# Kernel optimization log

Measured on AMD Instinct MI355X. Metric: run time of the kernel, lower is better.

The kernel has to match this reference:

```python
import jax, jax.numpy as jnp
import numpy as np

S, B, E, H = 2048, 2, 1024, 16
D = E // H  # head dim = 64


def setup_inputs() -> dict:
    key = jax.random.key(0)
    k1, k2, k3 = jax.random.split(key, 3)
    x = jax.random.normal(k1, (S, B, E), dtype=jnp.float32)
    Wqkv = jax.random.normal(k2, (3 * E, E), dtype=jnp.float32) * (E ** -0.5)
    bqkv = jax.random.normal(k3, (3 * E,), dtype=jnp.float32) * 0.02
    return {"x": x, "Wqkv": Wqkv, "bqkv": bqkv}


def reference(x, Wqkv, bqkv):
    s, b, e = x.shape
    h, d = H, E // H
    # fused QKV projection: [S,B,E] @ [E,3E] -> [S,B,3E]
    qkv = jnp.einsum('sbe,fe->sbf', x, Wqkv) + bqkv
    q, k, v = jnp.split(qkv, 3, axis=-1)
    q = q.reshape(s, b, h, d)
    k = k.reshape(s, b, h, d)
    v = v.reshape(s, b, h, d)
    scale = 1.0 / jnp.sqrt(jnp.asarray(d, dtype=x.dtype))
    # scores: [B,H,S,S]
    scores = jnp.einsum('sbhd,tbhd->bhst', q, k) * scale
    attn = jax.nn.softmax(scores, axis=-1)
    # context: [S,B,H,D] -> [S,B,E]
    ctx = jnp.einsum('bhst,tbhd->sbhd', attn, v)
    return ctx.reshape(s, b, e)
```

## Files before the change

### kernel.cpp

```cpp
#include <hip/hip_runtime.h>

constexpr int SEQ   = 2048;
constexpr int BATCH = 2;
constexpr int EMB   = 1024;
constexpr int NH    = 16;
constexpr int HDIM  = 64;
constexpr int MROWS = SEQ * BATCH;
constexpr int KDIM  = EMB;
constexpr int NCOLS = 3 * EMB;

typedef __bf16 bf16x8 __attribute__((ext_vector_type(8)));
typedef __bf16 bf16x4 __attribute__((ext_vector_type(4)));
typedef float  f32x4  __attribute__((ext_vector_type(4)));
typedef float  f32x16 __attribute__((ext_vector_type(16)));
typedef unsigned int u32;
typedef unsigned int u32x4 __attribute__((ext_vector_type(4)));

__device__ __forceinline__ u32 cvt_pk_bf16(float lo, float hi) {
  u32 r;
  asm("v_cvt_pk_bf16_f32 %0, %1, %2" : "=v"(r) : "v"(lo), "v"(hi));
  return r;
}
__device__ __forceinline__ void pl32_swap(u32& a, u32& b) {
  asm("v_permlane32_swap_b32 %0, %1" : "+v"(a), "+v"(b));
}
__device__ __forceinline__ void g2l16(const __bf16* g, __bf16* l) {
  __builtin_amdgcn_global_load_lds(
      (const __attribute__((address_space(1))) void*)g,
      (__attribute__((address_space(3))) void*)l, 16, 0, 0);
}

__global__ __launch_bounds__(256) void cvt_f32_bf16(
    const float* __restrict__ src, __bf16* __restrict__ dst, int n4) {
  int stride = gridDim.x * blockDim.x;
  for (int i = blockIdx.x * blockDim.x + threadIdx.x; i < n4; i += stride) {
    float4 v = reinterpret_cast<const float4*>(src)[i];
    bf16x4 o;
    o[0] = (__bf16)v.x; o[1] = (__bf16)v.y; o[2] = (__bf16)v.z; o[3] = (__bf16)v.w;
    reinterpret_cast<bf16x4*>(dst)[i] = o;
  }
}

__global__ __launch_bounds__(256) void qkv_gemm(
    const __bf16* __restrict__ Xb, const __bf16* __restrict__ Wb,
    const float* __restrict__ bqkv,
    __bf16* __restrict__ Qb, __bf16* __restrict__ Kb, __bf16* __restrict__ Vt) {
  __shared__ __attribute__((aligned(16))) __bf16 Al[128 * 64];
  __shared__ __attribute__((aligned(16))) __bf16 Bl[128 * 64];

  const int tid  = threadIdx.x;
  const int lane = tid & 63;
  const int w    = tid >> 6;
  const int wm   = w >> 1, wn = w & 1;
  const int m0   = blockIdx.y * 128;
  const int n0   = blockIdx.x * 128;

  f32x4 acc[4][4] = {};

  for (int kt = 0; kt < KDIM / 64; ++kt) {
    const int k0 = kt * 64;
    __syncthreads();
#pragma unroll
    for (int c = 0; c < 4; ++c) {
      const int u   = (w * 4 + c) * 64 + lane;
      const int row = u >> 3;
      const int sc  = ((u & 7) * 8) ^ ((row & 7) << 3);
      g2l16(&Xb[(size_t)(m0 + row) * KDIM + k0 + sc], Al + (w * 4 + c) * 512);
      g2l16(&Wb[(size_t)(n0 + row) * KDIM + k0 + sc], Bl + (w * 4 + c) * 512);
    }
    __syncthreads();

#pragma unroll
    for (int s = 0; s < 2; ++s) {
      bf16x8 af[4], bfr[4];
#pragma unroll
      for (int i = 0; i < 4; ++i) {
        const int ra = wm * 64 + i * 16 + (lane & 15);
        const int rb = wn * 64 + i * 16 + (lane & 15);
        const int colb = s * 32 + (lane >> 4) * 8;
        af[i]  = *reinterpret_cast<const bf16x8*>(&Al[ra * 64 + (colb ^ ((ra & 7) << 3))]);
        bfr[i] = *reinterpret_cast<const bf16x8*>(&Bl[rb * 64 + (colb ^ ((rb & 7) << 3))]);
      }
#pragma unroll
      for (int i = 0; i < 4; ++i)
#pragma unroll
        for (int j = 0; j < 4; ++j)
          acc[i][j] = __builtin_amdgcn_mfma_f32_16x16x32_bf16(af[i], bfr[j], acc[i][j], 0, 0, 0);
    }
  }

  const float QSCALE = 0.18033688011112042f;
#pragma unroll
  for (int j = 0; j < 4; ++j) {
    const int f    = n0 + wn * 64 + j * 16 + (lane & 15);
    const float bias = bqkv[f];
    const int sec  = f >> 10;
    const int hd   = f & 1023;
    const int h    = hd >> 6, d = hd & 63;
#pragma unroll
    for (int i = 0; i < 4; ++i) {
#pragma unroll
      for (int r = 0; r < 4; ++r) {
        const int mm = m0 + wm * 64 + i * 16 + (lane >> 4) * 4 + r;
        const int s_ = mm >> 1, b_ = mm & 1;
        const int bh = b_ * NH + h;
        const float val = acc[i][j][r] + bias;
        if (sec == 0) {
          Qb[((size_t)bh * SEQ + s_) * HDIM + d] = (__bf16)(val * QSCALE);
        } else if (sec == 1) {
          Kb[((size_t)bh * SEQ + s_) * HDIM + d] = (__bf16)val;
        } else {
          Vt[((size_t)bh * HDIM + d) * SEQ + s_] = (__bf16)val;
        }
      }
    }
  }
}

__global__ __launch_bounds__(256) void attn_fwd(
    const __bf16* __restrict__ Qb, const __bf16* __restrict__ Kb,
    const __bf16* __restrict__ Vt, float* __restrict__ out) {
  __shared__ __attribute__((aligned(16))) __bf16 lds[16384];

  const int tid  = threadIdx.x;
  const int lane = tid & 63;
  const int w    = tid >> 6;
  const int lq   = lane & 31;
  const int hi   = lane >> 5;

  const int bid  = blockIdx.x;
  const int wgid = (bid & 7) * 64 + (bid >> 3);
  const int qi   = wgid & 15;
  const int bh   = wgid >> 4;
  const int b_   = bh >> 4, h = bh & 15;
  const int q0   = qi * 128 + w * 32;

  const __bf16* Qp = Qb + (size_t)bh * SEQ * HDIM;
  const __bf16* Kp = Kb + (size_t)bh * SEQ * HDIM;
  const __bf16* Vp = Vt + (size_t)bh * HDIM * SEQ;

  bf16x8 qf[4];
#pragma unroll
  for (int ks = 0; ks < 4; ++ks)
    qf[ks] = *reinterpret_cast<const bf16x8*>(&Qp[(size_t)(q0 + lq) * HDIM + ks * 16 + hi * 8]);

  f32x16 acc0 = {}, acc1 = {};
  float m = -1e30f, l = 0.f;

  auto stage = [&](int b, int t0) {
#pragma unroll
    for (int c = 0; c < 2; ++c) {
      const int u   = (w * 2 + c) * 64 + lane;
      const int row = u >> 3;
      const int sc  = ((u & 7) * 8) ^ ((row & 7) << 3);
      g2l16(Kp + (size_t)(t0 + row) * HDIM + sc, lds + b * 8192 + (w * 2 + c) * 512);
      g2l16(Vp + (size_t)row * SEQ + t0 + sc,    lds + b * 8192 + 4096 + (w * 2 + c) * 512);
    }
  };

  stage(0, 0);
  __syncthreads();
  int cur = 0;

  for (int t0 = 0; t0 < SEQ; t0 += 64) {
    if (t0 + 64 < SEQ) stage(cur ^ 1, t0 + 64);
    const __bf16* kb = lds + cur * 8192;
    const __bf16* vb = kb + 4096;

    f32x16 S0 = {}, S1 = {};
#pragma unroll
    for (int ks = 0; ks < 4; ++ks) {
      const int colb = ks * 16 + hi * 8;
      bf16x8 k0 = *reinterpret_cast<const bf16x8*>(&kb[lq * 64        + (colb ^ ((lq & 7) << 3))]);
      bf16x8 k1 = *reinterpret_cast<const bf16x8*>(&kb[(32 + lq) * 64 + (colb ^ ((lq & 7) << 3))]);
      S0 = __builtin_amdgcn_mfma_f32_32x32x16_bf16(k0, qf[ks], S0, 0, 0, 0);
      S1 = __builtin_amdgcn_mfma_f32_32x32x16_bf16(k1, qf[ks], S1, 0, 0, 0);
    }

    float pmax = S0[0];
#pragma unroll
    for (int i = 1; i < 16; ++i) pmax = fmaxf(pmax, S0[i]);
#pragma unroll
    for (int i = 0; i < 16; ++i) pmax = fmaxf(pmax, S1[i]);
    pmax = fmaxf(pmax, __shfl_xor(pmax, 32));
    const float mnew  = fmaxf(m, pmax);
    const float alpha = __builtin_amdgcn_exp2f(m - mnew);
    m = mnew;
    float rs = 0.f;
#pragma unroll
    for (int i = 0; i < 16; ++i) { S0[i] = __builtin_amdgcn_exp2f(S0[i] - mnew); rs += S0[i]; }
#pragma unroll
    for (int i = 0; i < 16; ++i) { S1[i] = __builtin_amdgcn_exp2f(S1[i] - mnew); rs += S1[i]; }
    l = l * alpha + rs;
#pragma unroll
    for (int i = 0; i < 16; ++i) { acc0[i] *= alpha; acc1[i] *= alpha; }

    bf16x8 pw[4];
    {
      auto mk = [&](const f32x16& P, bf16x8* dst) {
#pragma unroll
        for (int kk = 0; kk < 2; ++kk) {
          u32 a0 = cvt_pk_bf16(P[kk * 8 + 0], P[kk * 8 + 1]);
          u32 b0 = cvt_pk_bf16(P[kk * 8 + 4], P[kk * 8 + 5]);
          u32 a1 = cvt_pk_bf16(P[kk * 8 + 2], P[kk * 8 + 3]);
          u32 b1 = cvt_pk_bf16(P[kk * 8 + 6], P[kk * 8 + 7]);
          pl32_swap(a0, b0);
          pl32_swap(a1, b1);
          u32x4 wv; wv[0] = a0; wv[1] = a1; wv[2] = b0; wv[3] = b1;
          dst[kk] = __builtin_bit_cast(bf16x8, wv);
        }
      };
      mk(S0, &pw[0]);
      mk(S1, &pw[2]);
    }

#pragma unroll
    for (int ks = 0; ks < 4; ++ks) {
      const int colb = ks * 16 + hi * 8;
      bf16x8 v0 = *reinterpret_cast<const bf16x8*>(&vb[lq * 64        + (colb ^ ((lq & 7) << 3))]);
      bf16x8 v1 = *reinterpret_cast<const bf16x8*>(&vb[(32 + lq) * 64 + (colb ^ ((lq & 7) << 3))]);
      acc0 = __builtin_amdgcn_mfma_f32_32x32x16_bf16(v0, pw[ks], acc0, 0, 0, 0);
      acc1 = __builtin_amdgcn_mfma_f32_32x32x16_bf16(v1, pw[ks], acc1, 0, 0, 0);
    }

    __syncthreads();
    cur ^= 1;
  }

  l += __shfl_xor(l, 32);
  const float inv = 1.0f / l;
  const int s_ = q0 + lq;
  float* op = out + ((size_t)s_ * BATCH + b_) * EMB + h * HDIM;
#pragma unroll
  for (int rr = 0; rr < 4; ++rr) {
    float4 o0 = {acc0[4 * rr] * inv, acc0[4 * rr + 1] * inv,
                 acc0[4 * rr + 2] * inv, acc0[4 * rr + 3] * inv};
    *reinterpret_cast<float4*>(&op[8 * rr + 4 * hi]) = o0;
    float4 o1 = {acc1[4 * rr] * inv, acc1[4 * rr + 1] * inv,
                 acc1[4 * rr + 2] * inv, acc1[4 * rr + 3] * inv};
    *reinterpret_cast<float4*>(&op[8 * rr + 4 * hi + 32]) = o1;
  }
}

extern "C" void kernel_launch(void* const* d_in, const int* in_sizes, int n_in,
                              void* d_out, int out_size, void* d_ws, size_t ws_size,
                              hipStream_t stream) {
  (void)in_sizes; (void)n_in; (void)out_size; (void)ws_size;
  const float* x    = (const float*)d_in[0];
  const float* Wqkv = (const float*)d_in[1];
  const float* bias = (const float*)d_in[2];
  float* out = (float*)d_out;

  char* ws = (char*)d_ws;
  __bf16* Xb = (__bf16*)(ws);
  __bf16* Wb = (__bf16*)(ws + 8388608);
  __bf16* Qb = (__bf16*)(ws + 14680064);
  __bf16* Kb = (__bf16*)(ws + 23068672);
  __bf16* Vt = (__bf16*)(ws + 31457280);

  cvt_f32_bf16<<<dim3(1024), dim3(256), 0, stream>>>(x, Xb, (MROWS * KDIM) / 4);
  cvt_f32_bf16<<<dim3(768), dim3(256), 0, stream>>>(Wqkv, Wb, (NCOLS * KDIM) / 4);
  qkv_gemm<<<dim3(NCOLS / 128, MROWS / 128), dim3(256), 0, stream>>>(Xb, Wb, bias, Qb, Kb, Vt);
  attn_fwd<<<dim3(512), dim3(256), 0, stream>>>(Qb, Kb, Vt, out);
}
```

Before: 126.1 us.

## Double-buffer QKV GEMM, shrink attention blocks, add lazy rescale and priorities

The QKV GEMM now uses a double-buffered 32-wide K loop with a new LDS swizzle, XCD-aware block remapping, setprio around MFMAs, and a single barrier per iteration. Attention moves to 128-thread blocks covering 64 queries, giving 1024 blocks with each wave staging more of K/V. It also adds setprio around the MFMA phases, tree max/sum reductions, and a lazy max rescale that skips the alpha update unless the max grows by more than 8 (log2 units). The goal is better load/compute overlap and more occupancy. Smaller attention blocks double K/V LDS traffic per query, and the lazy rescale lets exponents reach up to 2^8 before the correction is applied.

```diff
diff --git a/kernel.cpp b/kernel.cpp
--- a/kernel.cpp
+++ b/kernel.cpp
@@ -41,58 +41,68 @@
   }
 }
 
-__global__ __launch_bounds__(256) void qkv_gemm(
+__global__ __launch_bounds__(256, 4) void qkv_gemm(
     const __bf16* __restrict__ Xb, const __bf16* __restrict__ Wb,
     const float* __restrict__ bqkv,
     __bf16* __restrict__ Qb, __bf16* __restrict__ Kb, __bf16* __restrict__ Vt) {
-  __shared__ __attribute__((aligned(16))) __bf16 Al[128 * 64];
-  __shared__ __attribute__((aligned(16))) __bf16 Bl[128 * 64];
+  __shared__ __attribute__((aligned(16))) __bf16 Al[2][128 * 32];
+  __shared__ __attribute__((aligned(16))) __bf16 Bl[2][128 * 32];
 
   const int tid  = threadIdx.x;
   const int lane = tid & 63;
   const int w    = tid >> 6;
   const int wm   = w >> 1, wn = w & 1;
-  const int m0   = blockIdx.y * 128;
-  const int n0   = blockIdx.x * 128;
+
+  const int bid  = blockIdx.x;
+  const int wgid = (bid & 7) * 96 + (bid >> 3);
+  const int nx   = wgid % 24;
+  const int nyy  = wgid / 24;
+  const int m0   = nyy * 128;
+  const int n0   = nx * 128;
 
   f32x4 acc[4][4] = {};
 
-  for (int kt = 0; kt < KDIM / 64; ++kt) {
-    const int k0 = kt * 64;
+  auto stage = [&](int buf, int kt) {
+#pragma unroll
+    for (int c = 0; c < 2; ++c) {
+      const int u   = (w * 2 + c) * 64 + lane;
+      const int row = u >> 2;
+      const int sc  = ((u & 3) ^ ((row >> 1) & 3)) * 8;
+      g2l16(&Xb[(size_t)(m0 + row) * KDIM + kt * 32 + sc], &Al[buf][(w * 2 + c) * 512]);
+      g2l16(&Wb[(size_t)(n0 + row) * KDIM + kt * 32 + sc], &Bl[buf][(w * 2 + c) * 512]);
+    }
+  };
+
+  stage(0, 0);
+  __syncthreads();
+
+  const int l15 = lane & 15, hi4 = lane >> 4;
+  const int cswz = (hi4 ^ ((l15 >> 1) & 3)) * 8;
+
+  for (int kt = 0; kt < KDIM / 32; ++kt) {
+    const int buf = kt & 1;
+    if (kt + 1 < KDIM / 32) stage(buf ^ 1, kt + 1);
+
+    bf16x8 af[4], bfr[4];
+#pragma unroll
+    for (int i = 0; i < 4; ++i) {
+      af[i]  = *reinterpret_cast<const bf16x8*>(&Al[buf][(wm * 64 + i * 16 + l15) * 32 + cswz]);
+      bfr[i] = *reinterpret_cast<const bf16x8*>(&Bl[buf][(wn * 64 + i * 16 + l15) * 32 + cswz]);
+    }
+    __builtin_amdgcn_s_setprio(1);
+#pragma unroll
+    for (int i = 0; i < 4; ++i)
+#pragma unroll
+      for (int j = 0; j < 4; ++j)
+        acc[i][j] = __builtin_amdgcn_mfma_f32_16x16x32_bf16(af[i], bfr[j], acc[i][j], 0, 0, 0);
+    __builtin_amdgcn_s_setprio(0);
     __syncthreads();
-#pragma unroll
-    for (int c = 0; c < 4; ++c) {
-      const int u   = (w * 4 + c) * 64 + lane;
-      const int row = u >> 3;
-      const int sc  = ((u & 7) * 8) ^ ((row & 7) << 3);
-      g2l16(&Xb[(size_t)(m0 + row) * KDIM + k0 + sc], Al + (w * 4 + c) * 512);
-      g2l16(&Wb[(size_t)(n0 + row) * KDIM + k0 + sc], Bl + (w * 4 + c) * 512);
-    }
-    __syncthreads();
-
-#pragma unroll
-    for (int s = 0; s < 2; ++s) {
-      bf16x8 af[4], bfr[4];
-#pragma unroll
-      for (int i = 0; i < 4; ++i) {
-        const int ra = wm * 64 + i * 16 + (lane & 15);
-        const int rb = wn * 64 + i * 16 + (lane & 15);
-        const int colb = s * 32 + (lane >> 4) * 8;
-        af[i]  = *reinterpret_cast<const bf16x8*>(&Al[ra * 64 + (colb ^ ((ra & 7) << 3))]);
-        bfr[i] = *reinterpret_cast<const bf16x8*>(&Bl[rb * 64 + (colb ^ ((rb & 7) << 3))]);
-      }
-#pragma unroll
-      for (int i = 0; i < 4; ++i)
-#pragma unroll
-        for (int j = 0; j < 4; ++j)
-          acc[i][j] = __builtin_amdgcn_mfma_f32_16x16x32_bf16(af[i], bfr[j], acc[i][j], 0, 0, 0);
-    }
   }
 
   const float QSCALE = 0.18033688011112042f;
 #pragma unroll
   for (int j = 0; j < 4; ++j) {
-    const int f    = n0 + wn * 64 + j * 16 + (lane & 15);
+    const int f    = n0 + wn * 64 + j * 16 + l15;
     const float bias = bqkv[f];
     const int sec  = f >> 10;
     const int hd   = f & 1023;
@@ -101,7 +111,7 @@
     for (int i = 0; i < 4; ++i) {
 #pragma unroll
       for (int r = 0; r < 4; ++r) {
-        const int mm = m0 + wm * 64 + i * 16 + (lane >> 4) * 4 + r;
+        const int mm = m0 + wm * 64 + i * 16 + hi4 * 4 + r;
         const int s_ = mm >> 1, b_ = mm & 1;
         const int bh = b_ * NH + h;
         const float val = acc[i][j][r] + bias;
@@ -117,7 +127,7 @@
   }
 }
 
-__global__ __launch_bounds__(256) void attn_fwd(
+__global__ __launch_bounds__(128, 4) void attn_fwd(
     const __bf16* __restrict__ Qb, const __bf16* __restrict__ Kb,
     const __bf16* __restrict__ Vt, float* __restrict__ out) {
   __shared__ __attribute__((aligned(16))) __bf16 lds[16384];
@@ -129,11 +139,11 @@
   const int hi   = lane >> 5;
 
   const int bid  = blockIdx.x;
-  const int wgid = (bid & 7) * 64 + (bid >> 3);
-  const int qi   = wgid & 15;
-  const int bh   = wgid >> 4;
+  const int wgid = (bid & 7) * 128 + (bid >> 3);
+  const int qi   = wgid & 31;
+  const int bh   = wgid >> 5;
   const int b_   = bh >> 4, h = bh & 15;
-  const int q0   = qi * 128 + w * 32;
+  const int q0   = qi * 64 + w * 32;
 
   const __bf16* Qp = Qb + (size_t)bh * SEQ * HDIM;
   const __bf16* Kp = Kb + (size_t)bh * SEQ * HDIM;
@@ -149,25 +159,26 @@
 
   auto stage = [&](int b, int t0) {
 #pragma unroll
-    for (int c = 0; c < 2; ++c) {
-      const int u   = (w * 2 + c) * 64 + lane;
+    for (int c = 0; c < 4; ++c) {
+      const int u   = (w * 4 + c) * 64 + lane;
       const int row = u >> 3;
       const int sc  = ((u & 7) * 8) ^ ((row & 7) << 3);
-      g2l16(Kp + (size_t)(t0 + row) * HDIM + sc, lds + b * 8192 + (w * 2 + c) * 512);
-      g2l16(Vp + (size_t)row * SEQ + t0 + sc,    lds + b * 8192 + 4096 + (w * 2 + c) * 512);
+      g2l16(Kp + (size_t)(t0 + row) * HDIM + sc, lds + b * 8192 + (w * 4 + c) * 512);
+      g2l16(Vp + (size_t)row * SEQ + t0 + sc,    lds + b * 8192 + 4096 + (w * 4 + c) * 512);
     }
   };
 
   stage(0, 0);
   __syncthreads();
-  int cur = 0;
 
   for (int t0 = 0; t0 < SEQ; t0 += 64) {
+    const int cur = (t0 >> 6) & 1;
     if (t0 + 64 < SEQ) stage(cur ^ 1, t0 + 64);
     const __bf16* kb = lds + cur * 8192;
     const __bf16* vb = kb + 4096;
 
     f32x16 S0 = {}, S1 = {};
+    __builtin_amdgcn_s_setprio(1);
 #pragma unroll
     for (int ks = 0; ks < 4; ++ks) {
       const int colb = ks * 16 + hi * 8;
@@ -176,24 +187,51 @@
       S0 = __builtin_amdgcn_mfma_f32_32x32x16_bf16(k0, qf[ks], S0, 0, 0, 0);
       S1 = __builtin_amdgcn_mfma_f32_32x32x16_bf16(k1, qf[ks], S1, 0, 0, 0);
     }
-
-    float pmax = S0[0];
-#pragma unroll
-    for (int i = 1; i < 16; ++i) pmax = fmaxf(pmax, S0[i]);
-#pragma unroll
-    for (int i = 0; i < 16; ++i) pmax = fmaxf(pmax, S1[i]);
+    __builtin_amdgcn_s_setprio(0);
+
+    float pmax;
+    {
+      float t0m = fmaxf(S0[0], S0[1]), t1m = fmaxf(S0[2], S0[3]);
+      float t2m = fmaxf(S0[4], S0[5]), t3m = fmaxf(S0[6], S0[7]);
+      float t4m = fmaxf(S0[8], S0[9]), t5m = fmaxf(S0[10], S0[11]);
+      float t6m = fmaxf(S0[12], S0[13]), t7m = fmaxf(S0[14], S0[15]);
+      t0m = fmaxf(t0m, t1m); t2m = fmaxf(t2m, t3m); t4m = fmaxf(t4m, t5m); t6m = fmaxf(t6m, t7m);
+      float a_ = fmaxf(fmaxf(t0m, t2m), fmaxf(t4m, t6m));
+      float u0 = fmaxf(S1[0], S1[1]), u1 = fmaxf(S1[2], S1[3]);
+      float u2 = fmaxf(S1[4], S1[5]), u3 = fmaxf(S1[6], S1[7]);
+      float u4 = fmaxf(S1[8], S1[9]), u5 = fmaxf(S1[10], S1[11]);
+      float u6 = fmaxf(S1[12], S1[13]), u7 = fmaxf(S1[14], S1[15]);
+      u0 = fmaxf(u0, u1); u2 = fmaxf(u2, u3); u4 = fmaxf(u4, u5); u6 = fmaxf(u6, u7);
+      float b2 = fmaxf(fmaxf(u0, u2), fmaxf(u4, u6));
+      pmax = fmaxf(a_, b2);
+    }
     pmax = fmaxf(pmax, __shfl_xor(pmax, 32));
-    const float mnew  = fmaxf(m, pmax);
-    const float alpha = __builtin_amdgcn_exp2f(m - mnew);
-    m = mnew;
-    float rs = 0.f;
-#pragma unroll
-    for (int i = 0; i < 16; ++i) { S0[i] = __builtin_amdgcn_exp2f(S0[i] - mnew); rs += S0[i]; }
-#pragma unroll
-    for (int i = 0; i < 16; ++i) { S1[i] = __builtin_amdgcn_exp2f(S1[i] - mnew); rs += S1[i]; }
-    l = l * alpha + rs;
-#pragma unroll
-    for (int i = 0; i < 16; ++i) { acc0[i] *= alpha; acc1[i] *= alpha; }
+
+    if (__any(pmax > m + 8.f)) {
+      const float mnew  = fmaxf(m, pmax);
+      const float alpha = __builtin_amdgcn_exp2f(m - mnew);
+      m = mnew;
+      l *= alpha;
+#pragma unroll
+      for (int i = 0; i < 16; ++i) { acc0[i] *= alpha; acc1[i] *= alpha; }
+    }
+
+    float r0 = 0.f, r1 = 0.f, r2 = 0.f, r3 = 0.f;
+#pragma unroll
+    for (int i = 0; i < 4; ++i) {
+      S0[i]      = __builtin_amdgcn_exp2f(S0[i] - m);      r0 += S0[i];
+      S0[i + 4]  = __builtin_amdgcn_exp2f(S0[i + 4] - m);  r1 += S0[i + 4];
+      S0[i + 8]  = __builtin_amdgcn_exp2f(S0[i + 8] - m);  r2 += S0[i + 8];
+      S0[i + 12] = __builtin_amdgcn_exp2f(S0[i + 12] - m); r3 += S0[i + 12];
+    }
+#pragma unroll
+    for (int i = 0; i < 4; ++i) {
+      S1[i]      = __builtin_amdgcn_exp2f(S1[i] - m);      r0 += S1[i];
+      S1[i + 4]  = __builtin_amdgcn_exp2f(S1[i + 4] - m);  r1 += S1[i + 4];
+      S1[i + 8]  = __builtin_amdgcn_exp2f(S1[i + 8] - m);  r2 += S1[i + 8];
+      S1[i + 12] = __builtin_amdgcn_exp2f(S1[i + 12] - m); r3 += S1[i + 12];
+    }
+    l += (r0 + r1) + (r2 + r3);
 
     bf16x8 pw[4];
     {
@@ -214,6 +252,7 @@
       mk(S1, &pw[2]);
     }
 
+    __builtin_amdgcn_s_setprio(1);
 #pragma unroll
     for (int ks = 0; ks < 4; ++ks) {
       const int colb = ks * 16 + hi * 8;
@@ -222,9 +261,9 @@
       acc0 = __builtin_amdgcn_mfma_f32_32x32x16_bf16(v0, pw[ks], acc0, 0, 0, 0);
       acc1 = __builtin_amdgcn_mfma_f32_32x32x16_bf16(v1, pw[ks], acc1, 0, 0, 0);
     }
+    __builtin_amdgcn_s_setprio(0);
 
     __syncthreads();
-    cur ^= 1;
   }
 
   l += __shfl_xor(l, 32);
@@ -260,6 +299,6 @@
 
   cvt_f32_bf16<<<dim3(1024), dim3(256), 0, stream>>>(x, Xb, (MROWS * KDIM) / 4);
   cvt_f32_bf16<<<dim3(768), dim3(256), 0, stream>>>(Wqkv, Wb, (NCOLS * KDIM) / 4);
-  qkv_gemm<<<dim3(NCOLS / 128, MROWS / 128), dim3(256), 0, stream>>>(Xb, Wb, bias, Qb, Kb, Vt);
-  attn_fwd<<<dim3(512), dim3(256), 0, stream>>>(Qb, Kb, Vt, out);
-}
+  qkv_gemm<<<dim3(768), dim3(256), 0, stream>>>(Xb, Wb, bias, Qb, Kb, Vt);
+  attn_fwd<<<dim3(1024), dim3(128), 0, stream>>>(Qb, Kb, Vt, out);
+}
```

After: 115.4 us. -8.5%, faster.
